# Optimization experiments

Hardware: AMD Instinct MI355X
Metric: run time of the kernel (lower is better)

Reference implementation:

```python
import jax, jax.numpy as jnp
import numpy as np

B, C, L = 8, 256, 2048
RED = 8
CQK = C // RED  # 32


def setup_inputs() -> dict:
    key = jax.random.key(0)
    ks = jax.random.split(key, 8)
    s = 0.05
    x = jax.random.normal(ks[0], (B, C, L), dtype=jnp.float32)
    Wq = jax.random.normal(ks[1], (CQK, C), dtype=jnp.float32) * s
    bq = jax.random.normal(ks[2], (CQK,), dtype=jnp.float32) * s
    Wk = jax.random.normal(ks[3], (CQK, C), dtype=jnp.float32) * s
    bk = jax.random.normal(ks[4], (CQK,), dtype=jnp.float32) * s
    Wv = jax.random.normal(ks[5], (C, C), dtype=jnp.float32) * s
    bv = jax.random.normal(ks[6], (C,), dtype=jnp.float32) * s
    gamma = jnp.asarray([0.5], dtype=jnp.float32)  # learned scalar (init 0 in torch)
    return {"x": x, "Wq": Wq, "bq": bq, "Wk": Wk, "bk": bk, "Wv": Wv, "bv": bv, "gamma": gamma}


def reference(x, Wq, bq, Wk, bk, Wv, bv, gamma):
    # 1x1 Conv1d == channel-mixing matmul: [O,C] x [B,C,L] -> [B,O,L]
    q = jnp.einsum('oc,bcl->bol', Wq, x) + bq[:, None]   # [B,CQK,L]
    k = jnp.einsum('oc,bcl->bol', Wk, x) + bk[:, None]   # [B,CQK,L]
    v = jnp.einsum('oc,bcl->bol', Wv, x) + bv[:, None]   # [B,C,L]
    # attn[b,i,j] = softmax_j( q(:,i) . k(:,j) )  -- NOTE: no 1/sqrt(d) scaling
    scores = jnp.einsum('bci,bcj->bij', q, k)            # [B,L,L]
    attn = jax.nn.softmax(scores, axis=-1)
    # out[b,c,i] = sum_j v[b,c,j] * attn[b,i,j]
    out = jnp.einsum('bcj,bij->bci', v, attn)            # [B,C,L]
    return gamma[0] * out + x
```

## Files before the change

### kernel.cpp

```cpp
#include <hip/hip_runtime.h>

#define B 8
#define C 256
#define L 2048
#define CQK 32
#define SSEG 4
#define JSEG (L / SSEG)
#define NT (JSEG / 32)
#define SM_SHIFT2 28.8539008f

typedef unsigned short u16;
typedef __attribute__((ext_vector_type(8))) short bf8;
typedef __attribute__((ext_vector_type(4))) float f4;

__device__ __forceinline__ u16 f2bf(float f) {
    union { float f; unsigned u; } v; v.f = f;
    unsigned r = v.u + 0x7FFFu + ((v.u >> 16) & 1u);
    return (u16)(r >> 16);
}
__device__ __forceinline__ float bfl(unsigned u) {
    union { unsigned u; float f; } v; v.u = u << 16; return v.f;
}
__device__ __forceinline__ float bfh(unsigned u) {
    union { unsigned u; float f; } v; v.u = u & 0xFFFF0000u; return v.f;
}
__device__ __forceinline__ float ex2(float x) {
    float r;
    asm("v_exp_f32 %0, %1" : "=v"(r) : "v"(x));
    return r;
}

__device__ __forceinline__ void gld16(const u16* gp, u16* lp) {
    auto* g1 = (const __attribute__((address_space(1))) u16*)gp;
    auto* l3 = (__attribute__((address_space(3))) u16*)lp;
    __builtin_amdgcn_global_load_lds(g1, l3, 16, 0, 0);
}
__device__ __forceinline__ void wait_vm0() {
    asm volatile("s_waitcnt vmcnt(0)" ::: "memory");
    __builtin_amdgcn_sched_barrier(0);
}
__device__ __forceinline__ void wait_lgkm0() {
    asm volatile("s_waitcnt lgkmcnt(0)" ::: "memory");
    __builtin_amdgcn_sched_barrier(0);
}
__device__ __forceinline__ void bar() {
    __builtin_amdgcn_sched_barrier(0);
    __builtin_amdgcn_s_barrier();
    __builtin_amdgcn_sched_barrier(0);
}

__global__ __launch_bounds__(256) void wconv(
    const float* __restrict__ Wq, const float* __restrict__ bq,
    const float* __restrict__ Wk, const float* __restrict__ bk,
    const float* __restrict__ Wv, const float* __restrict__ bv,
    u16* __restrict__ Wall, float* __restrict__ ball)
{
    const int idx = (blockIdx.x * 256 + threadIdx.x) * 4;
    const int row = idx >> 8, c = idx & 255;
    const float* s;
    if (row < 32)      s = Wq + row * C + c;
    else if (row < 64) s = Wk + (row - 32) * C + c;
    else               s = Wv + (row - 64) * C + c;
    const float4 v = *(const float4*)s;
    uint2 o;
    o.x = f2bf(v.x) | ((unsigned)f2bf(v.y) << 16);
    o.y = f2bf(v.z) | ((unsigned)f2bf(v.w) << 16);
    *(uint2*)(Wall + idx) = o;
    if (blockIdx.x == 0) {
        for (int i = threadIdx.x; i < 320; i += 256)
            ball[i] = (i < 32) ? bq[i] : (i < 64) ? bk[i - 32] : bv[i - 64];
    }
}

__global__ __launch_bounds__(256) void xconv(const float* __restrict__ x,
                                             u16* __restrict__ xt)
{
    __shared__ float tile[64][65];
    const int b = blockIdx.z, c0 = blockIdx.y * 64, l0 = blockIdx.x * 64;
    const int t = threadIdx.x;
    const int ln = t & 63, w = t >> 6;
#pragma unroll
    for (int i = 0; i < 16; i++) {
        const int c = w * 16 + i;
        tile[c][ln] = x[((size_t)(b * C + c0 + c)) * L + l0 + ln];
    }
    __syncthreads();
    const int lrow = t >> 2, q = t & 3;
    unsigned o[8];
#pragma unroll
    for (int jj = 0; jj < 8; jj++) {
        const float a0 = tile[q * 16 + jj * 2][lrow];
        const float a1 = tile[q * 16 + jj * 2 + 1][lrow];
        o[jj] = f2bf(a0) | ((unsigned)f2bf(a1) << 16);
    }
    u16* dst = xt + ((size_t)(b * L + l0 + lrow)) * 256 + c0 + q * 16;
    *(uint4*)(dst)     = make_uint4(o[0], o[1], o[2], o[3]);
    *(uint4*)(dst + 8) = make_uint4(o[4], o[5], o[6], o[7]);
}

__global__ __launch_bounds__(256) void proj(
    const u16* __restrict__ xt, const u16* __restrict__ Wall,
    const float* __restrict__ ball, u16* __restrict__ qt,
    u16* __restrict__ kt, u16* __restrict__ vv)
{
    __shared__ u16 xlds[32 * 256];
    const int b = blockIdx.y, l0 = blockIdx.x * 32;
    const int t = threadIdx.x, w = t >> 6, ln = t & 63;
    const int lc = ln & 15, g = ln >> 4;

#pragma unroll
    for (int mm = 0; mm < 4; mm++) {
        const int cg = t + mm * 256;
        const int lrow = cg >> 5, phys = cg & 31;
        const int logical = (phys & 24) | ((phys & 7) ^ (lrow & 7));
        gld16(xt + ((size_t)(b * L + l0 + lrow)) * 256 + logical * 8,
              xlds + (size_t)(w * 64 + mm * 256) * 8);
    }
    __syncthreads();

    f4 acc[5][2];
#pragma unroll
    for (int rt = 0; rt < 5; rt++) {
        const int row0 = (w * 5 + rt) * 16 + g * 4;
        const float4 bi = *(const float4*)(ball + row0);
#pragma unroll
        for (int ct = 0; ct < 2; ct++) {
            acc[rt][ct].x = bi.x; acc[rt][ct].y = bi.y;
            acc[rt][ct].z = bi.z; acc[rt][ct].w = bi.w;
        }
    }

#pragma unroll
    for (int k = 0; k < 8; k++) {
        bf8 bfr[2];
#pragma unroll
        for (int ct = 0; ct < 2; ct++) {
            const int lrow = ct * 16 + lc;
            const int lchunk = k * 4 + g;
            const int phys = (lchunk & 24) | ((lchunk & 7) ^ (lrow & 7));
            bfr[ct] = *(const bf8*)(xlds + (size_t)lrow * 256 + phys * 8);
        }
#pragma unroll
        for (int rt = 0; rt < 5; rt++) {
            const bf8 af = *(const bf8*)(Wall +
                (size_t)((w * 5 + rt) * 16 + lc) * 256 + k * 32 + g * 8);
#pragma unroll
            for (int ct = 0; ct < 2; ct++)
                acc[rt][ct] = __builtin_amdgcn_mfma_f32_16x16x32_bf16(
                    af, bfr[ct], acc[rt][ct], 0, 0, 0);
        }
    }

    const float Q_SCALE = 1.44269504f;
#pragma unroll
    for (int rt = 0; rt < 5; rt++) {
        const int rg = w * 5 + rt;
        const int row0 = rg * 16 + g * 4;
#pragma unroll
        for (int ct = 0; ct < 2; ct++) {
            const int l = l0 + ct * 16 + lc;
            const f4 a = acc[rt][ct];
            if (rg < 2) {
                uint2 o;
                o.x = f2bf(a.x * Q_SCALE) | ((unsigned)f2bf(a.y * Q_SCALE) << 16);
                o.y = f2bf(a.z * Q_SCALE) | ((unsigned)f2bf(a.w * Q_SCALE) << 16);
                *(uint2*)(qt + ((size_t)(b * L + l)) * 32 + row0) = o;
            } else if (rg < 4) {
                uint2 o;
                o.x = f2bf(a.x) | ((unsigned)f2bf(a.y) << 16);
                o.y = f2bf(a.z) | ((unsigned)f2bf(a.w) << 16);
                *(uint2*)(kt + ((size_t)(b * L + l)) * 32 + (row0 - 32)) = o;
            } else {
                const int c = row0 - 64;
                vv[((size_t)(b * C + c + 0)) * L + l] = f2bf(a.x);
                vv[((size_t)(b * C + c + 1)) * L + l] = f2bf(a.y);
                vv[((size_t)(b * C + c + 2)) * L + l] = f2bf(a.z);
                vv[((size_t)(b * C + c + 3)) * L + l] = f2bf(a.w);
            }
        }
    }
}

__global__ __launch_bounds__(256, 4) void attn(
    const u16* __restrict__ qt, const u16* __restrict__ kt,
    const u16* __restrict__ vv, u16* __restrict__ po,
    float* __restrict__ plsum)
{
    __shared__ u16 vs[2][8192];
    __shared__ u16 ps[64][40];
    __shared__ float fl[64];

    const int fid = blockIdx.x;
    const int win = fid & 31, bx = fid >> 5;
    const int b = win >> 2, sidx = win & 3;
    const int t = threadIdx.x, w = t >> 6, ln = t & 63;
    const int lc = ln & 15, g = ln >> 4;
    const int i0 = bx * 64;
    const int js = sidx * JSEG;
    const int wc0 = w * 64;
    const int tb = (b * 32 + bx) * SSEG + sidx;

    const bf8 qf = *(const bf8*)(qt + ((size_t)(b * L + i0 + w * 16 + lc)) * 32 + g * 8);
    const u16* kb = kt + ((size_t)(b * L + js + lc)) * 32 + g * 8;

    const int sc = t >> 2, ss = t & 3;
    const u16* vsrc = vv + ((size_t)(b * C + sc)) * L + js + ((ss ^ (sc & 3)) * 8);

    f4 acc[4][4];
    const f4 fz = {0.f, 0.f, 0.f, 0.f};
#pragma unroll
    for (int it = 0; it < 4; it++)
#pragma unroll
        for (int ct = 0; ct < 4; ct++) acc[it][ct] = fz;
    float lsum = 0.f;

    auto stage = [&](int buf, int jt) {
        const u16* s = vsrc + jt * 32;
        u16* d = &vs[buf][0] + (size_t)(w * 64) * 8;
#pragma unroll
        for (int m = 0; m < 4; m++)
            gld16(s + (size_t)(m * 64) * L, d + (size_t)(m * 256) * 8);
    };

    stage(0, 0);
    bf8 kf0 = *(const bf8*)(kb);
    bf8 kf1 = *(const bf8*)(kb + 16 * 32);
    int cur = 0;

#pragma unroll 1
    for (int jt = 0; jt < NT; jt++) {
        wait_vm0();
        bar();
        if (jt + 1 < NT) stage(cur ^ 1, jt + 1);
        bf8 kn0 = kf0, kn1 = kf1;
        if (jt + 1 < NT) {
            kn0 = *(const bf8*)(kb + (size_t)((jt + 1) * 32) * 32);
            kn1 = *(const bf8*)(kb + (size_t)((jt + 1) * 32 + 16) * 32);
        }

        const f4 s0 = __builtin_amdgcn_mfma_f32_16x16x32_bf16(kf0, qf, fz, 0, 0, 0);
        const f4 s1 = __builtin_amdgcn_mfma_f32_16x16x32_bf16(kf1, qf, fz, 0, 0, 0);

        const float p0 = ex2(s0.x - SM_SHIFT2);
        const float p1 = ex2(s0.y - SM_SHIFT2);
        const float p2 = ex2(s0.z - SM_SHIFT2);
        const float p3 = ex2(s0.w - SM_SHIFT2);
        const float p4 = ex2(s1.x - SM_SHIFT2);
        const float p5 = ex2(s1.y - SM_SHIFT2);
        const float p6 = ex2(s1.z - SM_SHIFT2);
        const float p7 = ex2(s1.w - SM_SHIFT2);
        {
            uint2 o;
            o.x = f2bf(p0) | ((unsigned)f2bf(p1) << 16);
            o.y = f2bf(p2) | ((unsigned)f2bf(p3) << 16);
            *(uint2*)(&ps[w * 16 + lc][g * 4]) = o;
            o.x = f2bf(p4) | ((unsigned)f2bf(p5) << 16);
            o.y = f2bf(p6) | ((unsigned)f2bf(p7) << 16);
            *(uint2*)(&ps[w * 16 + lc][16 + g * 4]) = o;
        }
        float psum = ((p0 + p1) + (p2 + p3)) + ((p4 + p5) + (p6 + p7));
        psum += __shfl_xor(psum, 16);
        psum += __shfl_xor(psum, 32);
        lsum += psum;

        wait_lgkm0();
        bar();

        __builtin_amdgcn_s_setprio(1);
#pragma unroll
        for (int ct = 0; ct < 4; ct++) {
            const int c = wc0 + ct * 16 + lc;
            const bf8 vfr = *(const bf8*)(&vs[cur][0] + (size_t)c * 32 + ((g ^ (c & 3)) * 8));
#pragma unroll
            for (int it = 0; it < 4; it++) {
                const bf8 paf = *(const bf8*)(&ps[it * 16 + lc][0] + g * 8);
                acc[it][ct] = __builtin_amdgcn_mfma_f32_16x16x32_bf16(
                    paf, vfr, acc[it][ct], 0, 0, 0);
            }
        }
        __builtin_amdgcn_s_setprio(0);

        kf0 = kn0; kf1 = kn1;
        cur ^= 1;
    }

    fl[w * 16 + lc] = 1.0f / lsum;
    if (g == 0) plsum[(size_t)tb * 64 + w * 16 + lc] = lsum;
    wait_lgkm0();
    bar();
    u16* pob = po + ((size_t)tb * 2048 + t) * 8;
#pragma unroll
    for (int it = 0; it < 4; it++) {
        const float4 iv = *(const float4*)&fl[it * 16 + g * 4];
#pragma unroll
        for (int cp = 0; cp < 2; cp++) {
            const f4 a0 = acc[it][2 * cp];
            const f4 a1 = acc[it][2 * cp + 1];
            uint4 o;
            o.x = f2bf(a0.x * iv.x) | ((unsigned)f2bf(a0.y * iv.y) << 16);
            o.y = f2bf(a0.z * iv.z) | ((unsigned)f2bf(a0.w * iv.w) << 16);
            o.z = f2bf(a1.x * iv.x) | ((unsigned)f2bf(a1.y * iv.y) << 16);
            o.w = f2bf(a1.z * iv.z) | ((unsigned)f2bf(a1.w * iv.w) << 16);
            *(uint4*)(pob + (size_t)(it * 2 + cp) * 2048) = o;
        }
    }
}

__global__ __launch_bounds__(256) void combine(
    const u16* __restrict__ po, const float* __restrict__ plsum,
    const float* __restrict__ x, const float* __restrict__ gamma_p,
    float* __restrict__ out)
{
    __shared__ float raw[4][16];
    __shared__ float wts[4][16];
    const int bx = blockIdx.x, b = blockIdx.y, z = blockIdx.z;
    const int t = threadIdx.x, wq = t >> 6, ln = t & 63;
    const int lc = ln & 15, g = ln >> 4;
    const int tbase = (b * 32 + bx) * SSEG;

    if (t < 64)
        raw[t >> 4][t & 15] = plsum[(size_t)(tbase + (t >> 4)) * 64 + z * 16 + (t & 15)];
    __syncthreads();
    if (t < 16) {
        const float l0 = raw[0][t], l1 = raw[1][t], l2 = raw[2][t], l3 = raw[3][t];
        const float inv = 1.0f / (((l0 + l1) + (l2 + l3)));
        wts[0][t] = l0 * inv; wts[1][t] = l1 * inv;
        wts[2][t] = l2 * inv; wts[3][t] = l3 * inv;
    }
    __syncthreads();

    f4 tot[4];
    const f4 fz = {0.f, 0.f, 0.f, 0.f};
#pragma unroll
    for (int ct = 0; ct < 4; ct++) tot[ct] = fz;

#pragma unroll
    for (int s = 0; s < SSEG; s++) {
        const u16* base = po + ((size_t)(tbase + s) * 2048 + (size_t)z * 2 * 256 + t) * 8;
        const uint4 q0 = *(const uint4*)base;
        const uint4 q1 = *(const uint4*)(base + 2048);
        const float4 wv = *(const float4*)&wts[s][g * 4];
        tot[0].x += wv.x * bfl(q0.x); tot[0].y += wv.y * bfh(q0.x);
        tot[0].z += wv.z * bfl(q0.y); tot[0].w += wv.w * bfh(q0.y);
        tot[1].x += wv.x * bfl(q0.z); tot[1].y += wv.y * bfh(q0.z);
        tot[1].z += wv.z * bfl(q0.w); tot[1].w += wv.w * bfh(q0.w);
        tot[2].x += wv.x * bfl(q1.x); tot[2].y += wv.y * bfh(q1.x);
        tot[2].z += wv.z * bfl(q1.y); tot[2].w += wv.w * bfh(q1.y);
        tot[3].x += wv.x * bfl(q1.z); tot[3].y += wv.y * bfh(q1.z);
        tot[3].z += wv.z * bfl(q1.w); tot[3].w += wv.w * bfh(q1.w);
    }

    const float gmm = gamma_p[0];
#pragma unroll
    for (int ct = 0; ct < 4; ct++) {
        const int c = wq * 64 + ct * 16 + lc;
        const size_t adr = ((size_t)(b * C + c)) * L + bx * 64 + z * 16 + g * 4;
        const float4 xv = *(const float4*)(x + adr);
        float4 o;
        o.x = gmm * tot[ct].x + xv.x;
        o.y = gmm * tot[ct].y + xv.y;
        o.z = gmm * tot[ct].z + xv.z;
        o.w = gmm * tot[ct].w + xv.w;
        *(float4*)(out + adr) = o;
    }
}

extern "C" void kernel_launch(void* const* d_in, const int* in_sizes, int n_in,
                              void* d_out, int out_size, void* d_ws, size_t ws_size,
                              hipStream_t stream) {
    const float* x  = (const float*)d_in[0];
    const float* Wq = (const float*)d_in[1];
    const float* bq = (const float*)d_in[2];
    const float* Wk = (const float*)d_in[3];
    const float* bk = (const float*)d_in[4];
    const float* Wv = (const float*)d_in[5];
    const float* bv = (const float*)d_in[6];
    const float* gm = (const float*)d_in[7];
    float* out = (float*)d_out;

    u16* vvp  = (u16*)d_ws;
    u16* qtp  = vvp + (size_t)B * C * L;
    u16* ktp  = qtp + (size_t)B * L * CQK;
    u16* Wall = ktp + (size_t)B * L * CQK;
    float* ball = (float*)(Wall + 320 * 256);
    u16* xt   = Wall + 320 * 256 + 640;
    u16* po   = xt;
    float* plsum = (float*)(po + (size_t)B * 32 * SSEG * 2048 * 8);

    wconv<<<80, 256, 0, stream>>>(Wq, bq, Wk, bk, Wv, bv, Wall, ball);
    xconv<<<dim3(L / 64, C / 64, B), 256, 0, stream>>>(x, xt);
    proj<<<dim3(L / 32, B), 256, 0, stream>>>(xt, Wall, ball, qtp, ktp, vvp);
    attn<<<1024, 256, 0, stream>>>(qtp, ktp, vvp, po, plsum);
    combine<<<dim3(L / 64, B, SSEG), 256, 0, stream>>>(po, plsum, x, gm, out);
}
```

Baseline: 70.67 us.

## Split attention block across eight waves with per-wave V staging and packed bf16 converts

Doubles the attn block to 512 threads. Each of 8 waves now owns 32 output channels, with a private double-buffered V tile in LDS using an XOR swizzle. Only the first four waves compute scores and softmax probabilities, which all waves read from shared LDS. Manual bf16 rounding is replaced with the hardware v_cvt_pk_bf16_f32 instruction. The goal is more waves to hide latency and less per-wave accumulator pressure. The cost is idle score waves in half the block, a heavier block barrier, and a changed output layout that must still match combine.

```diff
diff --git a/kernel.cpp b/kernel.cpp
--- a/kernel.cpp
+++ b/kernel.cpp
@@ -23,6 +23,11 @@
 }
 __device__ __forceinline__ float bfh(unsigned u) {
     union { unsigned u; float f; } v; v.u = u & 0xFFFF0000u; return v.f;
+}
+__device__ __forceinline__ unsigned cvtpk(float lo, float hi) {
+    unsigned r;
+    asm("v_cvt_pk_bf16_f32 %0, %1, %2" : "=v"(r) : "v"(lo), "v"(hi));
+    return r;
 }
 __device__ __forceinline__ float ex2(float x) {
     float r;
@@ -181,12 +186,12 @@
     }
 }
 
-__global__ __launch_bounds__(256, 4) void attn(
+__global__ __launch_bounds__(512, 4) void attn(
     const u16* __restrict__ qt, const u16* __restrict__ kt,
     const u16* __restrict__ vv, u16* __restrict__ po,
     float* __restrict__ plsum)
 {
-    __shared__ u16 vs[2][8192];
+    __shared__ u16 vsw[8][2][1024];
     __shared__ u16 ps[64][40];
     __shared__ float fl[64];
 
@@ -197,80 +202,83 @@
     const int lc = ln & 15, g = ln >> 4;
     const int i0 = bx * 64;
     const int js = sidx * JSEG;
-    const int wc0 = w * 64;
+    const int wc0 = w * 32;
     const int tb = (b * 32 + bx) * SSEG + sidx;
 
-    const bf8 qf = *(const bf8*)(qt + ((size_t)(b * L + i0 + w * 16 + lc)) * 32 + g * 8);
-    const u16* kb = kt + ((size_t)(b * L + js + lc)) * 32 + g * 8;
-
-    const int sc = t >> 2, ss = t & 3;
-    const u16* vsrc = vv + ((size_t)(b * C + sc)) * L + js + ((ss ^ (sc & 3)) * 8);
-
-    f4 acc[4][4];
+    const int r0 = ln >> 2, s0 = ln & 3;
+    const int gch = s0 ^ (r0 & 3) ^ ((r0 >> 2) & 3);
+    const u16* vsrc = vv + ((size_t)(b * C + wc0 + r0)) * L + js + gch * 8;
+
+    f4 acc[4][2];
     const f4 fz = {0.f, 0.f, 0.f, 0.f};
 #pragma unroll
     for (int it = 0; it < 4; it++)
 #pragma unroll
-        for (int ct = 0; ct < 4; ct++) acc[it][ct] = fz;
+        for (int ct = 0; ct < 2; ct++) acc[it][ct] = fz;
     float lsum = 0.f;
+
+    bf8 qf = {}, kf0 = {}, kf1 = {}, kn0 = {}, kn1 = {};
+    const u16* kb = kt;
+    if (w < 4) {
+        qf = *(const bf8*)(qt + ((size_t)(b * L + i0 + w * 16 + lc)) * 32 + g * 8);
+        kb = kt + ((size_t)(b * L + js + lc)) * 32 + g * 8;
+        kn0 = *(const bf8*)(kb);
+        kn1 = *(const bf8*)(kb + 16 * 32);
+    }
 
     auto stage = [&](int buf, int jt) {
         const u16* s = vsrc + jt * 32;
-        u16* d = &vs[buf][0] + (size_t)(w * 64) * 8;
-#pragma unroll
-        for (int m = 0; m < 4; m++)
-            gld16(s + (size_t)(m * 64) * L, d + (size_t)(m * 256) * 8);
+        u16* d = &vsw[w][buf][0];
+        gld16(s, d);
+        gld16(s + (size_t)16 * L, d + 512);
     };
 
     stage(0, 0);
-    bf8 kf0 = *(const bf8*)(kb);
-    bf8 kf1 = *(const bf8*)(kb + 16 * 32);
     int cur = 0;
+
+    const int sread = (g ^ (lc & 3) ^ ((lc >> 2) & 3)) * 8;
 
 #pragma unroll 1
     for (int jt = 0; jt < NT; jt++) {
         wait_vm0();
         bar();
         if (jt + 1 < NT) stage(cur ^ 1, jt + 1);
-        bf8 kn0 = kf0, kn1 = kf1;
-        if (jt + 1 < NT) {
-            kn0 = *(const bf8*)(kb + (size_t)((jt + 1) * 32) * 32);
-            kn1 = *(const bf8*)(kb + (size_t)((jt + 1) * 32 + 16) * 32);
-        }
-
-        const f4 s0 = __builtin_amdgcn_mfma_f32_16x16x32_bf16(kf0, qf, fz, 0, 0, 0);
-        const f4 s1 = __builtin_amdgcn_mfma_f32_16x16x32_bf16(kf1, qf, fz, 0, 0, 0);
-
-        const float p0 = ex2(s0.x - SM_SHIFT2);
-        const float p1 = ex2(s0.y - SM_SHIFT2);
-        const float p2 = ex2(s0.z - SM_SHIFT2);
-        const float p3 = ex2(s0.w - SM_SHIFT2);
-        const float p4 = ex2(s1.x - SM_SHIFT2);
-        const float p5 = ex2(s1.y - SM_SHIFT2);
-        const float p6 = ex2(s1.z - SM_SHIFT2);
-        const float p7 = ex2(s1.w - SM_SHIFT2);
-        {
-            uint2 o;
-            o.x = f2bf(p0) | ((unsigned)f2bf(p1) << 16);
-            o.y = f2bf(p2) | ((unsigned)f2bf(p3) << 16);
-            *(uint2*)(&ps[w * 16 + lc][g * 4]) = o;
-            o.x = f2bf(p4) | ((unsigned)f2bf(p5) << 16);
-            o.y = f2bf(p6) | ((unsigned)f2bf(p7) << 16);
-            *(uint2*)(&ps[w * 16 + lc][16 + g * 4]) = o;
-        }
-        float psum = ((p0 + p1) + (p2 + p3)) + ((p4 + p5) + (p6 + p7));
-        psum += __shfl_xor(psum, 16);
-        psum += __shfl_xor(psum, 32);
-        lsum += psum;
+
+        if (w < 4) {
+            kf0 = kn0; kf1 = kn1;
+            if (jt + 1 < NT) {
+                kn0 = *(const bf8*)(kb + (size_t)((jt + 1) * 32) * 32);
+                kn1 = *(const bf8*)(kb + (size_t)((jt + 1) * 32 + 16) * 32);
+            }
+            const f4 sA = __builtin_amdgcn_mfma_f32_16x16x32_bf16(kf0, qf, fz, 0, 0, 0);
+            const f4 sB = __builtin_amdgcn_mfma_f32_16x16x32_bf16(kf1, qf, fz, 0, 0, 0);
+            const float p0 = ex2(sA.x - SM_SHIFT2);
+            const float p1 = ex2(sA.y - SM_SHIFT2);
+            const float p2 = ex2(sA.z - SM_SHIFT2);
+            const float p3 = ex2(sA.w - SM_SHIFT2);
+            const float p4 = ex2(sB.x - SM_SHIFT2);
+            const float p5 = ex2(sB.y - SM_SHIFT2);
+            const float p6 = ex2(sB.z - SM_SHIFT2);
+            const float p7 = ex2(sB.w - SM_SHIFT2);
+            uint2 oa, ob;
+            oa.x = cvtpk(p0, p1); oa.y = cvtpk(p2, p3);
+            ob.x = cvtpk(p4, p5); ob.y = cvtpk(p6, p7);
+            *(uint2*)(&ps[w * 16 + lc][g * 4]) = oa;
+            *(uint2*)(&ps[w * 16 + lc][16 + g * 4]) = ob;
+            float psum = ((p0 + p1) + (p2 + p3)) + ((p4 + p5) + (p6 + p7));
+            psum += __shfl_xor(psum, 16);
+            psum += __shfl_xor(psum, 32);
+            lsum += psum;
+        }
 
         wait_lgkm0();
         bar();
 
+        const u16* rb = &vsw[w][cur][0];
         __builtin_amdgcn_s_setprio(1);
 #pragma unroll
-        for (int ct = 0; ct < 4; ct++) {
-            const int c = wc0 + ct * 16 + lc;
-            const bf8 vfr = *(const bf8*)(&vs[cur][0] + (size_t)c * 32 + ((g ^ (c & 3)) * 8));
+        for (int ct = 0; ct < 2; ct++) {
+            const bf8 vfr = *(const bf8*)(rb + ct * 512 + lc * 32 + sread);
 #pragma unroll
             for (int it = 0; it < 4; it++) {
                 const bf8 paf = *(const bf8*)(&ps[it * 16 + lc][0] + g * 8);
@@ -279,30 +287,27 @@
             }
         }
         __builtin_amdgcn_s_setprio(0);
-
-        kf0 = kn0; kf1 = kn1;
         cur ^= 1;
     }
 
-    fl[w * 16 + lc] = 1.0f / lsum;
-    if (g == 0) plsum[(size_t)tb * 64 + w * 16 + lc] = lsum;
-    wait_lgkm0();
-    bar();
-    u16* pob = po + ((size_t)tb * 2048 + t) * 8;
+    if (w < 4) {
+        fl[w * 16 + lc] = 1.0f / lsum;
+        if (g == 0) plsum[(size_t)tb * 64 + w * 16 + lc] = lsum;
+    }
+    __syncthreads();
+    u16* pob = po + (size_t)tb * 16384 + (size_t)(w & 1) * 2048
+                  + ((size_t)(w >> 1) * 64 + g * 16 + lc) * 8;
 #pragma unroll
     for (int it = 0; it < 4; it++) {
         const float4 iv = *(const float4*)&fl[it * 16 + g * 4];
-#pragma unroll
-        for (int cp = 0; cp < 2; cp++) {
-            const f4 a0 = acc[it][2 * cp];
-            const f4 a1 = acc[it][2 * cp + 1];
-            uint4 o;
-            o.x = f2bf(a0.x * iv.x) | ((unsigned)f2bf(a0.y * iv.y) << 16);
-            o.y = f2bf(a0.z * iv.z) | ((unsigned)f2bf(a0.w * iv.w) << 16);
-            o.z = f2bf(a1.x * iv.x) | ((unsigned)f2bf(a1.y * iv.y) << 16);
-            o.w = f2bf(a1.z * iv.z) | ((unsigned)f2bf(a1.w * iv.w) << 16);
-            *(uint4*)(pob + (size_t)(it * 2 + cp) * 2048) = o;
-        }
+        const f4 a0 = acc[it][0];
+        const f4 a1 = acc[it][1];
+        uint4 o;
+        o.x = cvtpk(a0.x * iv.x, a0.y * iv.y);
+        o.y = cvtpk(a0.z * iv.z, a0.w * iv.w);
+        o.z = cvtpk(a1.x * iv.x, a1.y * iv.y);
+        o.w = cvtpk(a1.z * iv.z, a1.w * iv.w);
+        *(uint4*)(pob + (size_t)it * 4096) = o;
     }
 }
 
@@ -390,6 +395,6 @@
     wconv<<<80, 256, 0, stream>>>(Wq, bq, Wk, bk, Wv, bv, Wall, ball);
     xconv<<<dim3(L / 64, C / 64, B), 256, 0, stream>>>(x, xt);
     proj<<<dim3(L / 32, B), 256, 0, stream>>>(xt, Wall, ball, qtp, ktp, vvp);
-    attn<<<1024, 256, 0, stream>>>(qtp, ktp, vvp, po, plsum);
+    attn<<<1024, 512, 0, stream>>>(qtp, ktp, vvp, po, plsum);
     combine<<<dim3(L / 64, B, SSEG), 256, 0, stream>>>(po, plsum, x, gm, out);
 }
```

Result: slower. 77.73 us (+10.0%).
